# Kernel optimization log

Hardware: AMD Instinct MI355X
Metric: run time of the kernel (lower is better)

The kernel has to match this reference:

```python
import jax, jax.numpy as jnp
import numpy as np

B, Q, HID = 2, 2048, 2048
HQ, HKV, D = 16, 4, 128
EPS = 1e-6
THETA = 1000000.0


def _rmsnorm(x, w):
    # x: [..., D]
    return x * jax.lax.rsqrt(jnp.mean(x * x, axis=-1, keepdims=True) + EPS) * w


def _rope(x, cos, sin):
    # neox-style: split halves. x: [B,Q,H,D], cos/sin: [B,Q,1,D/2]
    d2 = x.shape[-1] // 2
    x1, x2 = x[..., :d2], x[..., d2:]
    return jnp.concatenate([x1 * cos - x2 * sin, x2 * cos + x1 * sin], axis=-1)


def setup_inputs() -> dict:
    key = jax.random.key(0)
    k1, k2, k3 = jax.random.split(key, 3)
    positions = jnp.broadcast_to(jnp.arange(Q, dtype=jnp.int32), (B, Q))
    hidden_states = jax.random.normal(k1, (B, Q, HID), dtype=jnp.float32)
    k_cache = jnp.zeros((B, HKV, Q, D), dtype=jnp.float32)
    v_cache = jnp.zeros((B, HKV, Q, D), dtype=jnp.float32)
    wqkv = jax.random.normal(k2, (HQ * D + 2 * HKV * D, HID), dtype=jnp.float32) * (HID ** -0.5)
    wo = jax.random.normal(k3, (HID, HQ * D), dtype=jnp.float32) * ((HQ * D) ** -0.5)
    q_norm_w = jnp.ones((D,), dtype=jnp.float32)
    k_norm_w = jnp.ones((D,), dtype=jnp.float32)
    return {"positions": positions, "hidden_states": hidden_states, "k_cache": k_cache,
            "v_cache": v_cache, "wqkv": wqkv, "wo": wo, "q_norm_w": q_norm_w,
            "k_norm_w": k_norm_w, "seq_len": Q}


def reference(positions, hidden_states, k_cache, v_cache, wqkv, wo, q_norm_w, k_norm_w, seq_len):
    bsz, qlen, _ = hidden_states.shape
    q_size, kv_size = HQ * D, HKV * D
    scale = D ** -0.5

    qkv = hidden_states.reshape(bsz * qlen, HID) @ wqkv.T  # [B*Q, q+2kv]
    q = qkv[:, :q_size].reshape(bsz, qlen, HQ, D)
    k = qkv[:, q_size:q_size + kv_size].reshape(bsz, qlen, HKV, D)
    v = qkv[:, q_size + kv_size:].reshape(bsz, qlen, HKV, D)

    q = _rmsnorm(q, q_norm_w)
    k = _rmsnorm(k, k_norm_w)

    inv_freq = 1.0 / (THETA ** (jnp.arange(0, D, 2, dtype=jnp.float32) / D))  # [D/2]
    freqs = positions.astype(jnp.float32)[..., None] * inv_freq  # [B,Q,D/2]
    cos = jnp.cos(freqs)[:, :, None, :]
    sin = jnp.sin(freqs)[:, :, None, :]
    q = _rope(q, cos, sin)
    k = _rope(k, cos, sin)

    q = q.transpose(0, 2, 1, 3)  # [B,HQ,Q,D]
    k = k.transpose(0, 2, 1, 3)  # [B,HKV,Q,D]
    v = v.transpose(0, 2, 1, 3)

    start = seq_len - qlen
    k_cache = jax.lax.dynamic_update_slice(k_cache, k, (0, 0, start, 0))
    v_cache = jax.lax.dynamic_update_slice(v_cache, v, (0, 0, start, 0))
    k_full = k_cache[:, :, :seq_len, :]
    v_full = v_cache[:, :, :seq_len, :]

    rep = HQ // HKV
    kf = jnp.repeat(k_full, rep, axis=1)  # [B,HQ,S,D]
    vf = jnp.repeat(v_full, rep, axis=1)

    scores = jnp.einsum('bhqd,bhkd->bhqk', q, kf) * scale
    if qlen == seq_len:  # is_causal path
        causal = jnp.tril(jnp.ones((qlen, seq_len), dtype=bool))
        scores = jnp.where(causal, scores, jnp.finfo(scores.dtype).min)
    attn = jax.nn.softmax(scores, axis=-1)
    out = jnp.einsum('bhqk,bhkd->bhqd', attn, vf)  # [B,HQ,Q,D]
    out = out.transpose(0, 2, 1, 3).reshape(bsz * qlen, HQ * D)
    return (out @ wo.T).reshape(bsz, qlen, HID)
```

## Files before the change

kernel.cpp:

```cpp
#include <hip/hip_runtime.h>

#define B_    2
#define Q_    2048
#define HID_  2048
#define HQ_   16
#define HKV_  4
#define D_    128
#define QSC_  (0.08838834764831843f * 1.4426950408889634f)
#define LOG2_THETA 19.931568569324174f
#define FMAX_ 20.0f

typedef unsigned short u16;
typedef __attribute__((ext_vector_type(8))) short bf16x8;
typedef __attribute__((ext_vector_type(4))) float f32x4;

__device__ __forceinline__ u16 f2bf(float x) {
  union { float f; unsigned int u; } v; v.f = x;
  unsigned int r = v.u + 0x7FFFu + ((v.u >> 16) & 1u);
  return (u16)(r >> 16);
}
__device__ __forceinline__ u16 f2bf_t(float x) {
  union { float f; unsigned int u; } v; v.f = x;
  return (u16)(v.u >> 16);
}

__device__ __forceinline__ void gl2lds16(u16* lds, const u16* g) {
  __builtin_amdgcn_global_load_lds((const __attribute__((address_space(1))) void*)g,
                                   (__attribute__((address_space(3))) void*)lds,
                                   16, 0, 0);
}

#define N4_HID  2097152
#define N4_WQKV 1572864
#define N4_WO   1048576
#define N4_ALL  (N4_HID + N4_WQKV + N4_WO)
#define NROPE   (B_ * Q_ * 64)
__global__ __launch_bounds__(256) void cvt_all(const float* __restrict__ h,
                                               const float* __restrict__ wq,
                                               const float* __restrict__ wo,
                                               const int* __restrict__ pos,
                                               u16* __restrict__ oh,
                                               u16* __restrict__ owq,
                                               u16* __restrict__ owo,
                                               float* __restrict__ rope) {
  int i = blockIdx.x * 256 + threadIdx.x;
  if (i >= N4_ALL) {
    int j = i - N4_ALL;
    int d = j & 63, row = j >> 6;
    float p = (float)pos[row];
    float inv = exp2f(-(float)d * (LOG2_THETA / 64.f));
    float sn, cn;
    sincosf(p * inv, &sn, &cn);
    ((float2*)rope)[j] = make_float2(cn, sn);
    return;
  }
  const float* src; u16* dst; int off;
  if (i < N4_HID)                 { src = h;  dst = oh;  off = i; }
  else if (i < N4_HID + N4_WQKV)  { src = wq; dst = owq; off = i - N4_HID; }
  else                            { src = wo; dst = owo; off = i - N4_HID - N4_WQKV; }
  float4 v = *(const float4*)(src + (size_t)off * 4);
  ushort4 o;
  o.x = f2bf(v.x); o.y = f2bf(v.y); o.z = f2bf(v.z); o.w = f2bf(v.w);
  *(ushort4*)(dst + (size_t)off * 4) = o;
}

__global__ __launch_bounds__(512) void gemm_qkv8(const u16* __restrict__ A,
                                                 const u16* __restrict__ Bw,
                                                 const float* __restrict__ rope,
                                                 const float* __restrict__ qw,
                                                 const float* __restrict__ kw,
                                                 u16* __restrict__ qb,
                                                 u16* __restrict__ kb,
                                                 u16* __restrict__ vt) {
  __shared__ __align__(16) u16 lds[65536];
  const int tid = threadIdx.x;
  const int wv = tid >> 6, lane = tid & 63;
  const int wm = wv >> 1, wn = wv & 1;
  const int c = lane & 15, quad = lane >> 4;
  const int m0 = blockIdx.x * 256;
  const int by = blockIdx.y;
  const int n0 = by * 256;
  const int xg = ((lane & 7) ^ (lane >> 3)) * 8;
  const int x0 = ((quad)     ^ (c & 7)) * 8;
  const int x1 = ((quad | 4) ^ (c & 7)) * 8;
  const int aoff = (wm >> 1) * 8192 + (wm & 1) * 4096 + c * 64;
  const int boff = 32768 + wn * 8192 + c * 64;
  const u16* Ag = A  + (size_t)m0 * HID_;
  const u16* Bg = Bw + (size_t)n0 * HID_;
  const int NIT = HID_ >> 7;

#define STGQ(base, g, h, kt, buf)                                             \
  { _Pragma("unroll")                                                         \
    for (int j = 0; j < 2; ++j) {                                             \
      const int s = j * 8 + wv;                                               \
      gl2lds16(lds + (base) + (buf) * 16384 + (h) * 8192 + s * 512,           \
               (g) + (size_t)((h) * 128 + s * 8 + (lane >> 3)) * HID_         \
                   + (kt) * 64 + xg);                                         \
    } }
#define STGQ_A(h, kt, buf) STGQ(0,     Ag, h, kt, buf)
#define STGQ_B(h, kt, buf) STGQ(32768, Bg, h, kt, buf)
#define BARQ()  asm volatile("s_barrier" ::: "memory")
#define WLGQ()  { asm volatile("s_waitcnt lgkmcnt(0)" ::: "memory");          \
                  __builtin_amdgcn_sched_barrier(0); }
#define WVMQ(n) { asm volatile("s_waitcnt vmcnt(" #n ")" ::: "memory");       \
                  __builtin_amdgcn_sched_barrier(0); }
#define MMQ(MF, NF, FA, MI) {                                                 \
  acc[MF][NF] = __builtin_amdgcn_mfma_f32_16x16x32_bf16(FA[MI][0], fB[(NF)&3][0], \
                                                        acc[MF][NF], 0, 0, 0);\
  acc[MF][NF] = __builtin_amdgcn_mfma_f32_16x16x32_bf16(FA[MI][1], fB[(NF)&3][1], \
                                                        acc[MF][NF], 0, 0, 0); }

  f32x4 acc[4][8] = {};
  bf16x8 fAa[2][2], fAb[2][2], fB[4][2];

  STGQ_A(0, 0, 0); STGQ_A(1, 0, 0); STGQ_B(0, 0, 0); STGQ_B(1, 0, 0);
  STGQ_A(0, 1, 1); STGQ_B(0, 1, 1);
  WVMQ(4);
  BARQ();

#pragma unroll 1
  for (int it = 0; it < NIT; ++it) {
    const bool last = (it == NIT - 1);
    const int kt1 = 2 * it + 1, kt2 = 2 * it + 2, kt3 = 2 * it + 3;

#pragma unroll
    for (int mi = 0; mi < 2; ++mi) {
      fAa[mi][0] = *(const bf16x8*)(lds + aoff + mi * 1024 + x0);
      fAa[mi][1] = *(const bf16x8*)(lds + aoff + mi * 1024 + x1);
    }
#pragma unroll
    for (int nf = 0; nf < 4; ++nf) {
      fB[nf][0] = *(const bf16x8*)(lds + boff + nf * 1024 + x0);
      fB[nf][1] = *(const bf16x8*)(lds + boff + nf * 1024 + x1);
    }
    STGQ_A(1, kt1, 1);
    BARQ(); WLGQ();
    __builtin_amdgcn_s_setprio(1);
#pragma unroll
    for (int mi = 0; mi < 2; ++mi)
#pragma unroll
      for (int nf = 0; nf < 4; ++nf) MMQ(mi, nf, fAa, mi);
    __builtin_amdgcn_s_setprio(0);
    BARQ();

#pragma unroll
    for (int mi = 0; mi < 2; ++mi) {
      fAb[mi][0] = *(const bf16x8*)(lds + aoff + (2 + mi) * 1024 + x0);
      fAb[mi][1] = *(const bf16x8*)(lds + aoff + (2 + mi) * 1024 + x1);
    }
    STGQ_B(1, kt1, 1);
    BARQ(); WLGQ();
    __builtin_amdgcn_s_setprio(1);
#pragma unroll
    for (int mi = 0; mi < 2; ++mi)
#pragma unroll
      for (int nf = 0; nf < 4; ++nf) MMQ(2 + mi, nf, fAb, mi);
    __builtin_amdgcn_s_setprio(0);
    BARQ();

#pragma unroll
    for (int nf = 0; nf < 4; ++nf) {
      fB[nf][0] = *(const bf16x8*)(lds + boff + (4 + nf) * 1024 + x0);
      fB[nf][1] = *(const bf16x8*)(lds + boff + (4 + nf) * 1024 + x1);
    }
    if (!last) STGQ_A(0, kt2, 0);
    BARQ(); WLGQ();
    __builtin_amdgcn_s_setprio(1);
#pragma unroll
    for (int mi = 0; mi < 2; ++mi)
#pragma unroll
      for (int nf = 4; nf < 8; ++nf) MMQ(2 + mi, nf, fAb, mi);
    __builtin_amdgcn_s_setprio(0);
    BARQ();

    if (!last) STGQ_B(0, kt2, 0);
    BARQ(); WLGQ();
    __builtin_amdgcn_s_setprio(1);
#pragma unroll
    for (int mi = 0; mi < 2; ++mi)
#pragma unroll
      for (int nf = 4; nf < 8; ++nf) MMQ(mi, nf, fAa, mi);
    __builtin_amdgcn_s_setprio(0);
    if (last) { WVMQ(0); } else { WVMQ(4); }
    BARQ();

#pragma unroll
    for (int mi = 0; mi < 2; ++mi) {
      fAa[mi][0] = *(const bf16x8*)(lds + 16384 + aoff + mi * 1024 + x0);
      fAa[mi][1] = *(const bf16x8*)(lds + 16384 + aoff + mi * 1024 + x1);
    }
#pragma unroll
    for (int nf = 0; nf < 4; ++nf) {
      fB[nf][0] = *(const bf16x8*)(lds + 16384 + boff + nf * 1024 + x0);
      fB[nf][1] = *(const bf16x8*)(lds + 16384 + boff + nf * 1024 + x1);
    }
    if (!last) STGQ_A(1, kt2, 0);
    BARQ(); WLGQ();
    __builtin_amdgcn_s_setprio(1);
#pragma unroll
    for (int mi = 0; mi < 2; ++mi)
#pragma unroll
      for (int nf = 0; nf < 4; ++nf) MMQ(mi, nf, fAa, mi);
    __builtin_amdgcn_s_setprio(0);
    BARQ();

#pragma unroll
    for (int mi = 0; mi < 2; ++mi) {
      fAb[mi][0] = *(const bf16x8*)(lds + 16384 + aoff + (2 + mi) * 1024 + x0);
      fAb[mi][1] = *(const bf16x8*)(lds + 16384 + aoff + (2 + mi) * 1024 + x1);
    }
    if (!last) STGQ_B(1, kt2, 0);
    BARQ(); WLGQ();
    __builtin_amdgcn_s_setprio(1);
#pragma unroll
    for (int mi = 0; mi < 2; ++mi)
#pragma unroll
      for (int nf = 0; nf < 4; ++nf) MMQ(2 + mi, nf, fAb, mi);
    __builtin_amdgcn_s_setprio(0);
    BARQ();

#pragma unroll
    for (int nf = 0; nf < 4; ++nf) {
      fB[nf][0] = *(const bf16x8*)(lds + 16384 + boff + (4 + nf) * 1024 + x0);
      fB[nf][1] = *(const bf16x8*)(lds + 16384 + boff + (4 + nf) * 1024 + x1);
    }
    if (!last) STGQ_A(0, kt3, 1);
    BARQ(); WLGQ();
    __builtin_amdgcn_s_setprio(1);
#pragma unroll
    for (int mi = 0; mi < 2; ++mi)
#pragma unroll
      for (int nf = 4; nf < 8; ++nf) MMQ(2 + mi, nf, fAb, mi);
    __builtin_amdgcn_s_setprio(0);
    BARQ();

    if (!last) STGQ_B(0, kt3, 1);
    BARQ(); WLGQ();
    __builtin_amdgcn_s_setprio(1);
#pragma unroll
    for (int mi = 0; mi < 2; ++mi)
#pragma unroll
      for (int nf = 4; nf < 8; ++nf) MMQ(mi, nf, fAa, mi);
    __builtin_amdgcn_s_setprio(0);
    if (last) { WVMQ(0); } else { WVMQ(4); }
    BARQ();
  }

  const int h = by * 2 + wn;
  if (h < 20) {
    const bool isq = h < 16;
    const float* w = isq ? qw : kw;
    const float osc = isq ? QSC_ : 1.f;
    float wl[8];
#pragma unroll
    for (int nf = 0; nf < 8; ++nf) wl[nf] = w[nf * 16 + c];
    u16* dstbuf = isq ? qb : kb;
    const int hbase = isq ? h : (h - 16);
    const int nheads = isq ? HQ_ : HKV_;
    u16* lw = lds + wv * 4224;
#pragma unroll
    for (int pass = 0; pass < 2; ++pass) {
#pragma unroll
      for (int mi = 0; mi < 2; ++mi) {
        const int mf = pass * 2 + mi;
#pragma unroll
        for (int r = 0; r < 4; ++r) {
          const int row = m0 + wm * 64 + mf * 16 + quad * 4 + r;
          const int q = row & (Q_ - 1), b = row >> 11;
          float ss = 0.f;
#pragma unroll
          for (int nf = 0; nf < 8; ++nf) ss += acc[mf][nf][r] * acc[mf][nf][r];
          ss += __shfl_xor(ss, 1); ss += __shfl_xor(ss, 2);
          ss += __shfl_xor(ss, 4); ss += __shfl_xor(ss, 8);
          const float rn = rsqrtf(ss * (1.f / 128.f) + 1e-6f) * osc;
          u16* lrow = lw + (mi * 16 + quad * 4 + r) * 132;
#pragma unroll
          for (int ni = 0; ni < 4; ni++) {
            float2 cssn = *(const float2*)(rope +
                ((size_t)(b * Q_ + q) * 64 + ni * 16 + c) * 2);
            float x1 = acc[mf][ni][r]     * wl[ni]     * rn;
            float x2 = acc[mf][ni + 4][r] * wl[ni + 4] * rn;
            lrow[ni * 16 + c]       = f2bf(x1 * cssn.x - x2 * cssn.y);
            lrow[(ni + 4) * 16 + c] = f2bf(x2 * cssn.x + x1 * cssn.y);
          }
        }
      }
#pragma unroll
      for (int itr = 0; itr < 8; ++itr) {
        const int rl = itr * 4 + quad;
        const int rowg = m0 + wm * 64 + pass * 32 + rl;
        const int q = rowg & (Q_ - 1), b = rowg >> 11;
        u16* dst = dstbuf + (((size_t)(b * nheads) + hbase) * Q_ + q) * D_ + c * 8;
        *(bf16x8*)dst = *(const bf16x8*)(lw + rl * 132 + c * 8);
      }
    }
  } else {
    const int hk = h - 20;
    const int bb = m0 >> 11;
    const int q0w = (m0 & (Q_ - 1)) + wm * 64;
    u16* lw = lds + wv * 4352;
#pragma unroll
    for (int pass = 0; pass < 2; ++pass) {
#pragma unroll
      for (int nfl = 0; nfl < 4; ++nfl) {
        const int nf = pass * 4 + nfl;
#pragma unroll
        for (int mf = 0; mf < 4; ++mf) {
          short4 pv;
          pv.x = (short)f2bf(acc[mf][nf][0]); pv.y = (short)f2bf(acc[mf][nf][1]);
          pv.z = (short)f2bf(acc[mf][nf][2]); pv.w = (short)f2bf(acc[mf][nf][3]);
          *(short4*)(lw + (nfl * 16 + c) * 68 + mf * 16 + quad * 4) = pv;
        }
      }
#pragma unroll
      for (int itr = 0; itr < 8; ++itr) {
        const int dl = itr * 8 + (lane >> 3);
        const int d = pass * 64 + dl;
        u16* dst = vt + (((size_t)(bb * HKV_) + hk) * D_ + d) * Q_ +
                   q0w + (lane & 7) * 8;
        *(bf16x8*)dst = *(const bf16x8*)(lw + dl * 68 + (lane & 7) * 8);
      }
    }
  }
#undef STGQ
#undef STGQ_A
#undef STGQ_B
#undef BARQ
#undef WLGQ
#undef WVMQ
#undef MMQ
}

__global__ __launch_bounds__(512) void gemm_bt8(const u16* __restrict__ A,
                                                const u16* __restrict__ Bw,
                                                float* __restrict__ C,
                                                int M, int N, int K) {
  __shared__ __align__(16) u16 lds[65536];
  const int tid = threadIdx.x;
  const int wv = tid >> 6, lane = tid & 63;
  const int wm = wv >> 2, wn = wv & 3;
  const int c = lane & 15, quad = lane >> 4;
  const int m0 = blockIdx.x * 256, n0 = blockIdx.y * 256;
  const int xg = ((lane & 7) ^ (lane >> 3)) * 8;
  const int x0 = ((quad)     ^ (c & 7)) * 8;
  const int x1 = ((quad | 4) ^ (c & 7)) * 8;
  const int aoff = wm * 8192 + c * 64;
  const int boff = 32768 + (wn >> 1) * 8192 + (wn & 1) * 4096 + c * 64;
  const u16* Ag = A  + (size_t)m0 * K;
  const u16* Bg = Bw + (size_t)n0 * K;
  const int NIT = K >> 7;

#define STG8(base, g, h, kt, buf)                                             \
  { _Pragma("unroll")                                                         \
    for (int j = 0; j < 2; ++j) {                                             \
      const int s = j * 8 + wv;                                               \
      gl2lds16(lds + (base) + (buf) * 16384 + (h) * 8192 + s * 512,           \
               (g) + (size_t)((h) * 128 + s * 8 + (lane >> 3)) * K            \
                   + (kt) * 64 + xg);                                         \
    } }
#define STG_A8(h, kt, buf) STG8(0,     Ag, h, kt, buf)
#define STG_B8(h, kt, buf) STG8(32768, Bg, h, kt, buf)
#define BAR8()  asm volatile("s_barrier" ::: "memory")
#define WLG8()  { asm volatile("s_waitcnt lgkmcnt(0)" ::: "memory");          \
                  __builtin_amdgcn_sched_barrier(0); }
#define WVM8(n) { asm volatile("s_waitcnt vmcnt(" #n ")" ::: "memory");       \
                  __builtin_amdgcn_sched_barrier(0); }
#define MFMA8(MF, NF, KS) acc[MF][NF] = __builtin_amdgcn_mfma_f32_16x16x32_bf16( \
                  fA[(MF) & 3][KS], fB[NF][KS], acc[MF][NF], 0, 0, 0)

  f32x4 acc[8][4] = {};
  bf16x8 fA[4][2], fB[4][2];

  STG_A8(0, 0, 0); STG_A8(1, 0, 0); STG_B8(0, 0, 0); STG_B8(1, 0, 0);
  STG_B8(0, 1, 1); STG_A8(0, 1, 1);
  WVM8(4);
  BAR8();

#pragma unroll 1
  for (int it = 0; it < NIT; ++it) {
    const bool last = (it == NIT - 1);
    const int kt1 = 2 * it + 1, kt2 = 2 * it + 2, kt3 = 2 * it + 3;

#pragma unroll
    for (int mf = 0; mf < 4; ++mf) {
      fA[mf][0] = *(const bf16x8*)(lds + aoff + mf * 1024 + x0);
      fA[mf][1] = *(const bf16x8*)(lds + aoff + mf * 1024 + x1);
    }
#pragma unroll
    for (int nf = 0; nf < 2; ++nf) {
      fB[nf][0] = *(const bf16x8*)(lds + boff + nf * 1024 + x0);
      fB[nf][1] = *(const bf16x8*)(lds + boff + nf * 1024 + x1);
    }
    STG_A8(1, kt1, 1);
    BAR8(); WLG8();
    __builtin_amdgcn_s_setprio(1);
#pragma unroll
    for (int mf = 0; mf < 4; ++mf)
#pragma unroll
      for (int nf = 0; nf < 2; ++nf) { MFMA8(mf, nf, 0); MFMA8(mf, nf, 1); }
    __builtin_amdgcn_s_setprio(0);
    BAR8();

#pragma unroll
    for (int nf = 2; nf < 4; ++nf) {
      fB[nf][0] = *(const bf16x8*)(lds + boff + nf * 1024 + x0);
      fB[nf][1] = *(const bf16x8*)(lds + boff + nf * 1024 + x1);
    }
    STG_B8(1, kt1, 1);
    BAR8(); WLG8();
    __builtin_amdgcn_s_setprio(1);
#pragma unroll
    for (int mf = 0; mf < 4; ++mf)
#pragma unroll
      for (int nf = 2; nf < 4; ++nf) { MFMA8(mf, nf, 0); MFMA8(mf, nf, 1); }
    __builtin_amdgcn_s_setprio(0);
    BAR8();

#pragma unroll
    for (int mf = 0; mf < 4; ++mf) {
      fA[mf][0] = *(const bf16x8*)(lds + aoff + (4 + mf) * 1024 + x0);
      fA[mf][1] = *(const bf16x8*)(lds + aoff + (4 + mf) * 1024 + x1);
    }
    if (!last) STG_B8(0, kt2, 0);
    BAR8(); WLG8();
    __builtin_amdgcn_s_setprio(1);
#pragma unroll
    for (int mf = 4; mf < 8; ++mf)
#pragma unroll
      for (int nf = 2; nf < 4; ++nf) { MFMA8(mf, nf, 0); MFMA8(mf, nf, 1); }
    __builtin_amdgcn_s_setprio(0);
    BAR8();

    if (!last) STG_A8(0, kt2, 0);
    BAR8(); WLG8();
    __builtin_amdgcn_s_setprio(1);
#pragma unroll
    for (int mf = 4; mf < 8; ++mf)
#pragma unroll
      for (int nf = 0; nf < 2; ++nf) { MFMA8(mf, nf, 0); MFMA8(mf, nf, 1); }
    __builtin_amdgcn_s_setprio(0);
    if (last) { WVM8(0); } else { WVM8(4); }
    BAR8();

#pragma unroll
    for (int mf = 0; mf < 4; ++mf) {
      fA[mf][0] = *(const bf16x8*)(lds + 16384 + aoff + mf * 1024 + x0);
      fA[mf][1] = *(const bf16x8*)(lds + 16384 + aoff + mf * 1024 + x1);
    }
#pragma unroll
    for (int nf = 0; nf < 2; ++nf) {
      fB[nf][0] = *(const bf16x8*)(lds + 16384 + boff + nf * 1024 + x0);
      fB[nf][1] = *(const bf16x8*)(lds + 16384 + boff + nf * 1024 + x1);
    }
    if (!last) STG_A8(1, kt2, 0);
    BAR8(); WLG8();
    __builtin_amdgcn_s_setprio(1);
#pragma unroll
    for (int mf = 0; mf < 4; ++mf)
#pragma unroll
      for (int nf = 0; nf < 2; ++nf) { MFMA8(mf, nf, 0); MFMA8(mf, nf, 1); }
    __builtin_amdgcn_s_setprio(0);
    BAR8();

#pragma unroll
    for (int nf = 2; nf < 4; ++nf) {
      fB[nf][0] = *(const bf16x8*)(lds + 16384 + boff + nf * 1024 + x0);
      fB[nf][1] = *(const bf16x8*)(lds + 16384 + boff + nf * 1024 + x1);
    }
    if (!last) STG_B8(1, kt2, 0);
    BAR8(); WLG8();
    __builtin_amdgcn_s_setprio(1);
#pragma unroll
    for (int mf = 0; mf < 4; ++mf)
#pragma unroll
      for (int nf = 2; nf < 4; ++nf) { MFMA8(mf, nf, 0); MFMA8(mf, nf, 1); }
    __builtin_amdgcn_s_setprio(0);
    BAR8();

#pragma unroll
    for (int mf = 0; mf < 4; ++mf) {
      fA[mf][0] = *(const bf16x8*)(lds + 16384 + aoff + (4 + mf) * 1024 + x0);
      fA[mf][1] = *(const bf16x8*)(lds + 16384 + aoff + (4 + mf) * 1024 + x1);
    }
    if (!last) STG_B8(0, kt3, 1);
    BAR8(); WLG8();
    __builtin_amdgcn_s_setprio(1);
#pragma unroll
    for (int mf = 4; mf < 8; ++mf)
#pragma unroll
      for (int nf = 2; nf < 4; ++nf) { MFMA8(mf, nf, 0); MFMA8(mf, nf, 1); }
    __builtin_amdgcn_s_setprio(0);
    BAR8();

    if (!last) STG_A8(0, kt3, 1);
    BAR8(); WLG8();
    __builtin_amdgcn_s_setprio(1);
#pragma unroll
    for (int mf = 4; mf < 8; ++mf)
#pragma unroll
      for (int nf = 0; nf < 2; ++nf) { MFMA8(mf, nf, 0); MFMA8(mf, nf, 1); }
    __builtin_amdgcn_s_setprio(0);
    if (last) { WVM8(0); } else { WVM8(4); }
    BAR8();
  }

  const int crow = m0 + wm * 128 + quad * 4;
  const int ccol = n0 + wn * 64 + c;
#pragma unroll
  for (int mf = 0; mf < 8; ++mf)
#pragma unroll
    for (int nf = 0; nf < 4; ++nf)
#pragma unroll
      for (int r = 0; r < 4; ++r)
        C[(size_t)(crow + mf * 16 + r) * N + ccol + nf * 16] = acc[mf][nf][r];
#undef STG8
#undef STG_A8
#undef STG_B8
#undef BAR8
#undef WLG8
#undef WVM8
#undef MFMA8
}

__global__ __launch_bounds__(256) void attn_fwd(const u16* __restrict__ qb,
                                                const u16* __restrict__ kb,
                                                const u16* __restrict__ vt,
                                                u16* __restrict__ ob) {
  __shared__ __align__(16) u16 lds[8192 + 8192 + 4608];
  u16* Ks = lds;
  u16* Vs = lds + 8192;
  u16* Ps = lds + 16384;
  const int p = blockIdx.x, h = blockIdx.y, b = blockIdx.z;
  const int hk = h >> 2;
  const int tid = threadIdx.x, wave = tid >> 6, lane = tid & 63;
  const int c = lane & 15, quad = lane >> 4;
  const int lr = lane >> 2, lp = lane & 3;
  const int lpg = (lp + 4 - ((lr >> 1) & 3)) & 3;
  const int swq = ((quad + (c >> 1)) & 3) * 8;
  const u16* qg = qb + ((size_t)b * HQ_ + h) * (size_t)Q_ * D_;
  const u16* kg = kb + ((size_t)b * HKV_ + hk) * (size_t)Q_ * D_;
  const u16* vg = vt + ((size_t)b * HKV_ + hk) * (size_t)D_ * Q_;
  u16* Pw = Ps + wave * 1152;
  u16* Bw = Ks + wave * 2176;

#pragma unroll 1
  for (int tp = 0; tp < 2; tp++) {
    const int t = tp ? (31 - p) : p;
    const int q0 = t * 64;
    const int qrow = q0 + wave * 16 + c;
    bf16x8 qf[4];
#pragma unroll
    for (int kk = 0; kk < 4; kk++)
      qf[kk] = *(const bf16x8*)(qg + (size_t)qrow * D_ + kk * 32 + quad * 8);
    f32x4 Oa[8] = {};
    float l_acc = 0.f;

#pragma unroll 1
    for (int kt = 0; kt <= t; kt++) {
      __syncthreads();
#pragma unroll
      for (int i = 0; i < 4; i++) {
        gl2lds16(Ks + (size_t)(i * 256 + wave * 64) * 8,
                 kg + ((size_t)kt * 64 + wave * 16 + lr) * D_ + i * 32 + lpg * 8);
        int d = (i & 1) * 64 + wave * 16 + lr;
        gl2lds16(Vs + (size_t)(i * 256 + wave * 64) * 8,
                 vg + (size_t)d * Q_ + kt * 64 + (i >> 1) * 32 + lpg * 8);
      }
      __syncthreads();
      f32x4 S[4];
#pragma unroll
      for (int n = 0; n < 4; n++) {
        f32x4 a = {-FMAX_, -FMAX_, -FMAX_, -FMAX_};
#pragma unroll
        for (int kk = 0; kk < 4; kk++) {
          bf16x8 kf = *(const bf16x8*)(Ks + kk * 2048 + (n * 16 + c) * 32 + swq);
          a = __builtin_amdgcn_mfma_f32_16x16x32_bf16(kf, qf[kk], a, 0, 0, 0);
        }
        S[n] = a;
      }
      if (kt == t) {
#pragma unroll
        for (int n = 0; n < 4; n++)
#pragma unroll
          for (int r = 0; r < 4; r++) {
            int key = kt * 64 + n * 16 + quad * 4 + r;
            if (key > qrow) S[n][r] = -1e9f;
          }
      }
#pragma unroll
      for (int n = 0; n < 4; n++) {
        float p0 = __builtin_amdgcn_exp2f(S[n][0]);
        float p1 = __builtin_amdgcn_exp2f(S[n][1]);
        float p2 = __builtin_amdgcn_exp2f(S[n][2]);
        float p3 = __builtin_amdgcn_exp2f(S[n][3]);
        l_acc += (p0 + p1) + (p2 + p3);
        short4 pk;
        pk.x = (short)f2bf_t(p0); pk.y = (short)f2bf_t(p1);
        pk.z = (short)f2bf_t(p2); pk.w = (short)f2bf_t(p3);
        *(short4*)(Pw + c * 72 + n * 16 + quad * 4) = pk;
      }
      bf16x8 pf[2];
#pragma unroll
      for (int kk2 = 0; kk2 < 2; kk2++)
        pf[kk2] = *(const bf16x8*)(Pw + c * 72 + kk2 * 32 + quad * 8);
#pragma unroll
      for (int md = 0; md < 8; md++)
#pragma unroll
        for (int kk2 = 0; kk2 < 2; kk2++) {
          bf16x8 vf = *(const bf16x8*)(Vs + kk2 * 4096 + (md * 16 + c) * 32 + swq);
          Oa[md] = __builtin_amdgcn_mfma_f32_16x16x32_bf16(vf, pf[kk2], Oa[md], 0, 0, 0);
        }
    }
    float l_row = l_acc;
    l_row += __shfl_xor(l_row, 16);
    l_row += __shfl_xor(l_row, 32);
    __syncthreads();
    const float invl = 1.f / l_row;
#pragma unroll
    for (int md = 0; md < 8; md++) {
      short4 ok;
      ok.x = (short)f2bf(Oa[md][0] * invl); ok.y = (short)f2bf(Oa[md][1] * invl);
      ok.z = (short)f2bf(Oa[md][2] * invl); ok.w = (short)f2bf(Oa[md][3] * invl);
      *(short4*)(Bw + c * 136 + md * 16 + quad * 4) = ok;
    }
    const int orow = q0 + wave * 16 + lr;
#pragma unroll
    for (int tt = 0; tt < 4; tt++) {
      bf16x8 ov = *(const bf16x8*)(Bw + lr * 136 + lp * 32 + tt * 8);
      *(bf16x8*)(ob + ((size_t)(b * Q_ + orow) * HQ_ + h) * D_ + lp * 32 + tt * 8) = ov;
    }
  }
}

extern "C" void kernel_launch(void* const* d_in, const int* in_sizes, int n_in,
                              void* d_out, int out_size, void* d_ws, size_t ws_size,
                              hipStream_t stream) {
  const int*   positions = (const int*)  d_in[0];
  const float* hidden    = (const float*)d_in[1];
  const float* wqkv      = (const float*)d_in[4];
  const float* wo        = (const float*)d_in[5];
  const float* qnw       = (const float*)d_in[6];
  const float* knw       = (const float*)d_in[7];
  char* ws = (char*)d_ws;
  u16*   hid_bf  = (u16*)(ws);
  u16*   wqkv_bf = (u16*)(ws + 16777216);
  u16*   wo_bf   = (u16*)(ws + 29360128);
  u16*   q_bf    = (u16*)(ws + 37748736);
  u16*   k_bf    = (u16*)(ws + 54525952);
  u16*   vt_bf   = (u16*)(ws + 58720256);
  float* rope    = (float*)(ws + 62914560);
  u16*   attn_bf = hid_bf;

  cvt_all<<<19456, 256, 0, stream>>>(hidden, wqkv, wo, positions,
                                     hid_bf, wqkv_bf, wo_bf, rope);
  gemm_qkv8<<<dim3(16, 12), 512, 0, stream>>>(hid_bf, wqkv_bf, rope, qnw, knw,
                                              q_bf, k_bf, vt_bf);
  attn_fwd<<<dim3(16, 16, 2), 256, 0, stream>>>(q_bf, k_bf, vt_bf, attn_bf);
  gemm_bt8<<<dim3(16, 8), 512, 0, stream>>>(attn_bf, wo_bf, (float*)d_out,
                                            4096, 2048, 2048);
}
```

Measured before the change: 309.1 us.

## Shrink output GEMM tile to 128x256 and double-buffer K/V loads in attention

The output projection GEMM moves from 256x256 tiles to 128x256 tiles, doubling the grid from 128 to 256 blocks so that more of the compute units have work. Its software pipeline is rebuilt with a smaller LDS footprint and split A/B fragment registers. The attention kernel now double-buffers its K and V tiles in LDS, prefetching the next tile while the current one is computed, which also removes one barrier per iteration. The cost is more LDS per attention block, which can lower occupancy, and less operand reuse per GEMM tile.

```diff
diff --git a/kernel.cpp b/kernel.cpp
--- a/kernel.cpp
+++ b/kernel.cpp
@@ -335,201 +335,173 @@
                                                 const u16* __restrict__ Bw,
                                                 float* __restrict__ C,
                                                 int M, int N, int K) {
-  __shared__ __align__(16) u16 lds[65536];
+  __shared__ __align__(16) u16 lds[49152];
   const int tid = threadIdx.x;
   const int wv = tid >> 6, lane = tid & 63;
   const int wm = wv >> 2, wn = wv & 3;
   const int c = lane & 15, quad = lane >> 4;
-  const int m0 = blockIdx.x * 256, n0 = blockIdx.y * 256;
+  const int m0 = blockIdx.x * 128, n0 = blockIdx.y * 256;
   const int xg = ((lane & 7) ^ (lane >> 3)) * 8;
   const int x0 = ((quad)     ^ (c & 7)) * 8;
   const int x1 = ((quad | 4) ^ (c & 7)) * 8;
-  const int aoff = wm * 8192 + c * 64;
-  const int boff = 32768 + (wn >> 1) * 8192 + (wn & 1) * 4096 + c * 64;
+  const int aoff = wm * 4096 + c * 64;
+  const int boff = 16384 + (wn >> 1) * 8192 + (wn & 1) * 4096 + c * 64;
   const u16* Ag = A  + (size_t)m0 * K;
   const u16* Bg = Bw + (size_t)n0 * K;
   const int NIT = K >> 7;
 
-#define STG8(base, g, h, kt, buf)                                             \
+#define STA2(h, kt, buf)                                                      \
+  gl2lds16(lds + (buf) * 8192 + (h) * 4096 + wv * 512,                        \
+           Ag + (size_t)((h) * 64 + wv * 8 + (lane >> 3)) * K + (kt) * 64 + xg);
+#define STB2(h, kt, buf)                                                      \
   { _Pragma("unroll")                                                         \
-    for (int j = 0; j < 2; ++j) {                                             \
-      const int s = j * 8 + wv;                                               \
-      gl2lds16(lds + (base) + (buf) * 16384 + (h) * 8192 + s * 512,           \
-               (g) + (size_t)((h) * 128 + s * 8 + (lane >> 3)) * K            \
-                   + (kt) * 64 + xg);                                         \
-    } }
-#define STG_A8(h, kt, buf) STG8(0,     Ag, h, kt, buf)
-#define STG_B8(h, kt, buf) STG8(32768, Bg, h, kt, buf)
+    for (int j = 0; j < 2; ++j)                                               \
+      gl2lds16(lds + 16384 + (buf) * 16384 + (h) * 8192 + j * 4096 + wv * 512,\
+               Bg + (size_t)((h) * 128 + j * 64 + wv * 8 + (lane >> 3)) * K   \
+                   + (kt) * 64 + xg); }
 #define BAR8()  asm volatile("s_barrier" ::: "memory")
 #define WLG8()  { asm volatile("s_waitcnt lgkmcnt(0)" ::: "memory");          \
                   __builtin_amdgcn_sched_barrier(0); }
 #define WVM8(n) { asm volatile("s_waitcnt vmcnt(" #n ")" ::: "memory");       \
                   __builtin_amdgcn_sched_barrier(0); }
-#define MFMA8(MF, NF, KS) acc[MF][NF] = __builtin_amdgcn_mfma_f32_16x16x32_bf16( \
-                  fA[(MF) & 3][KS], fB[NF][KS], acc[MF][NF], 0, 0, 0)
-
-  f32x4 acc[8][4] = {};
-  bf16x8 fA[4][2], fB[4][2];
-
-  STG_A8(0, 0, 0); STG_A8(1, 0, 0); STG_B8(0, 0, 0); STG_B8(1, 0, 0);
-  STG_B8(0, 1, 1); STG_A8(0, 1, 1);
-  WVM8(4);
+#define MM2(MF, NF, FA, FB, MI, NI) {                                         \
+  acc[MF][NF] = __builtin_amdgcn_mfma_f32_16x16x32_bf16(FA[MI][0], FB[NI][0], \
+                                                        acc[MF][NF], 0, 0, 0);\
+  acc[MF][NF] = __builtin_amdgcn_mfma_f32_16x16x32_bf16(FA[MI][1], FB[NI][1], \
+                                                        acc[MF][NF], 0, 0, 0); }
+
+  f32x4 acc[4][4] = {};
+  bf16x8 fAa[2][2], fAb[2][2], fBa[2][2], fBb[2][2];
+
+  STA2(0, 0, 0); STA2(1, 0, 0); STB2(0, 0, 0); STB2(1, 0, 0);
+  STA2(0, 1, 1); STA2(1, 1, 1); STB2(0, 1, 1); STB2(1, 1, 1);
+  WVM8(6);
   BAR8();
 
 #pragma unroll 1
   for (int it = 0; it < NIT; ++it) {
     const bool last = (it == NIT - 1);
-    const int kt1 = 2 * it + 1, kt2 = 2 * it + 2, kt3 = 2 * it + 3;
-
-#pragma unroll
-    for (int mf = 0; mf < 4; ++mf) {
-      fA[mf][0] = *(const bf16x8*)(lds + aoff + mf * 1024 + x0);
-      fA[mf][1] = *(const bf16x8*)(lds + aoff + mf * 1024 + x1);
-    }
-#pragma unroll
-    for (int nf = 0; nf < 2; ++nf) {
-      fB[nf][0] = *(const bf16x8*)(lds + boff + nf * 1024 + x0);
-      fB[nf][1] = *(const bf16x8*)(lds + boff + nf * 1024 + x1);
-    }
-    STG_A8(1, kt1, 1);
-    BAR8(); WLG8();
-    __builtin_amdgcn_s_setprio(1);
-#pragma unroll
-    for (int mf = 0; mf < 4; ++mf)
-#pragma unroll
-      for (int nf = 0; nf < 2; ++nf) { MFMA8(mf, nf, 0); MFMA8(mf, nf, 1); }
-    __builtin_amdgcn_s_setprio(0);
-    BAR8();
-
-#pragma unroll
-    for (int nf = 2; nf < 4; ++nf) {
-      fB[nf][0] = *(const bf16x8*)(lds + boff + nf * 1024 + x0);
-      fB[nf][1] = *(const bf16x8*)(lds + boff + nf * 1024 + x1);
-    }
-    STG_B8(1, kt1, 1);
-    BAR8(); WLG8();
-    __builtin_amdgcn_s_setprio(1);
-#pragma unroll
-    for (int mf = 0; mf < 4; ++mf)
-#pragma unroll
-      for (int nf = 2; nf < 4; ++nf) { MFMA8(mf, nf, 0); MFMA8(mf, nf, 1); }
-    __builtin_amdgcn_s_setprio(0);
-    BAR8();
-
-#pragma unroll
-    for (int mf = 0; mf < 4; ++mf) {
-      fA[mf][0] = *(const bf16x8*)(lds + aoff + (4 + mf) * 1024 + x0);
-      fA[mf][1] = *(const bf16x8*)(lds + aoff + (4 + mf) * 1024 + x1);
-    }
-    if (!last) STG_B8(0, kt2, 0);
-    BAR8(); WLG8();
-    __builtin_amdgcn_s_setprio(1);
-#pragma unroll
-    for (int mf = 4; mf < 8; ++mf)
-#pragma unroll
-      for (int nf = 2; nf < 4; ++nf) { MFMA8(mf, nf, 0); MFMA8(mf, nf, 1); }
-    __builtin_amdgcn_s_setprio(0);
-    BAR8();
-
-    if (!last) STG_A8(0, kt2, 0);
-    BAR8(); WLG8();
-    __builtin_amdgcn_s_setprio(1);
-#pragma unroll
-    for (int mf = 4; mf < 8; ++mf)
-#pragma unroll
-      for (int nf = 0; nf < 2; ++nf) { MFMA8(mf, nf, 0); MFMA8(mf, nf, 1); }
-    __builtin_amdgcn_s_setprio(0);
-    if (last) { WVM8(0); } else { WVM8(4); }
-    BAR8();
-
-#pragma unroll
-    for (int mf = 0; mf < 4; ++mf) {
-      fA[mf][0] = *(const bf16x8*)(lds + 16384 + aoff + mf * 1024 + x0);
-      fA[mf][1] = *(const bf16x8*)(lds + 16384 + aoff + mf * 1024 + x1);
-    }
-#pragma unroll
-    for (int nf = 0; nf < 2; ++nf) {
-      fB[nf][0] = *(const bf16x8*)(lds + 16384 + boff + nf * 1024 + x0);
-      fB[nf][1] = *(const bf16x8*)(lds + 16384 + boff + nf * 1024 + x1);
-    }
-    if (!last) STG_A8(1, kt2, 0);
-    BAR8(); WLG8();
-    __builtin_amdgcn_s_setprio(1);
-#pragma unroll
-    for (int mf = 0; mf < 4; ++mf)
-#pragma unroll
-      for (int nf = 0; nf < 2; ++nf) { MFMA8(mf, nf, 0); MFMA8(mf, nf, 1); }
-    __builtin_amdgcn_s_setprio(0);
-    BAR8();
-
-#pragma unroll
-    for (int nf = 2; nf < 4; ++nf) {
-      fB[nf][0] = *(const bf16x8*)(lds + 16384 + boff + nf * 1024 + x0);
-      fB[nf][1] = *(const bf16x8*)(lds + 16384 + boff + nf * 1024 + x1);
-    }
-    if (!last) STG_B8(1, kt2, 0);
-    BAR8(); WLG8();
-    __builtin_amdgcn_s_setprio(1);
-#pragma unroll
-    for (int mf = 0; mf < 4; ++mf)
-#pragma unroll
-      for (int nf = 2; nf < 4; ++nf) { MFMA8(mf, nf, 0); MFMA8(mf, nf, 1); }
-    __builtin_amdgcn_s_setprio(0);
-    BAR8();
-
-#pragma unroll
-    for (int mf = 0; mf < 4; ++mf) {
-      fA[mf][0] = *(const bf16x8*)(lds + 16384 + aoff + (4 + mf) * 1024 + x0);
-      fA[mf][1] = *(const bf16x8*)(lds + 16384 + aoff + (4 + mf) * 1024 + x1);
-    }
-    if (!last) STG_B8(0, kt3, 1);
-    BAR8(); WLG8();
-    __builtin_amdgcn_s_setprio(1);
-#pragma unroll
-    for (int mf = 4; mf < 8; ++mf)
-#pragma unroll
-      for (int nf = 2; nf < 4; ++nf) { MFMA8(mf, nf, 0); MFMA8(mf, nf, 1); }
-    __builtin_amdgcn_s_setprio(0);
-    BAR8();
-
-    if (!last) STG_A8(0, kt3, 1);
-    BAR8(); WLG8();
-    __builtin_amdgcn_s_setprio(1);
-#pragma unroll
-    for (int mf = 4; mf < 8; ++mf)
-#pragma unroll
-      for (int nf = 0; nf < 2; ++nf) { MFMA8(mf, nf, 0); MFMA8(mf, nf, 1); }
-    __builtin_amdgcn_s_setprio(0);
-    if (last) { WVM8(0); } else { WVM8(4); }
+    const int kt2 = 2 * it + 2, kt3 = 2 * it + 3;
+
+#pragma unroll
+    for (int mi = 0; mi < 2; ++mi) {
+      fAa[mi][0] = *(const bf16x8*)(lds + aoff + mi * 1024 + x0);
+      fAa[mi][1] = *(const bf16x8*)(lds + aoff + mi * 1024 + x1);
+      fBa[mi][0] = *(const bf16x8*)(lds + boff + mi * 1024 + x0);
+      fBa[mi][1] = *(const bf16x8*)(lds + boff + mi * 1024 + x1);
+    }
+    BAR8(); WLG8();
+    __builtin_amdgcn_s_setprio(1);
+    MM2(0, 0, fAa, fBa, 0, 0); MM2(0, 1, fAa, fBa, 0, 1);
+    MM2(1, 0, fAa, fBa, 1, 0); MM2(1, 1, fAa, fBa, 1, 1);
+    __builtin_amdgcn_s_setprio(0);
+    BAR8();
+
+#pragma unroll
+    for (int mi = 0; mi < 2; ++mi) {
+      fAb[mi][0] = *(const bf16x8*)(lds + aoff + (2 + mi) * 1024 + x0);
+      fAb[mi][1] = *(const bf16x8*)(lds + aoff + (2 + mi) * 1024 + x1);
+    }
+    BAR8(); WLG8();
+    __builtin_amdgcn_s_setprio(1);
+    MM2(2, 0, fAb, fBa, 0, 0); MM2(2, 1, fAb, fBa, 0, 1);
+    MM2(3, 0, fAb, fBa, 1, 0); MM2(3, 1, fAb, fBa, 1, 1);
+    __builtin_amdgcn_s_setprio(0);
+    BAR8();
+
+#pragma unroll
+    for (int ni = 0; ni < 2; ++ni) {
+      fBb[ni][0] = *(const bf16x8*)(lds + boff + (2 + ni) * 1024 + x0);
+      fBb[ni][1] = *(const bf16x8*)(lds + boff + (2 + ni) * 1024 + x1);
+    }
+    if (!last) { STA2(0, kt2, 0); STA2(1, kt2, 0); }
+    BAR8(); WLG8();
+    __builtin_amdgcn_s_setprio(1);
+    MM2(2, 2, fAb, fBb, 0, 0); MM2(2, 3, fAb, fBb, 0, 1);
+    MM2(3, 2, fAb, fBb, 1, 0); MM2(3, 3, fAb, fBb, 1, 1);
+    __builtin_amdgcn_s_setprio(0);
+    BAR8();
+
+    if (!last) { STB2(0, kt2, 0); STB2(1, kt2, 0); }
+    BAR8(); WLG8();
+    __builtin_amdgcn_s_setprio(1);
+    MM2(0, 2, fAa, fBb, 0, 0); MM2(0, 3, fAa, fBb, 0, 1);
+    MM2(1, 2, fAa, fBb, 1, 0); MM2(1, 3, fAa, fBb, 1, 1);
+    __builtin_amdgcn_s_setprio(0);
+    if (last) { WVM8(0); } else { WVM8(6); }
+    BAR8();
+
+#pragma unroll
+    for (int mi = 0; mi < 2; ++mi) {
+      fAa[mi][0] = *(const bf16x8*)(lds + 8192 + aoff + mi * 1024 + x0);
+      fAa[mi][1] = *(const bf16x8*)(lds + 8192 + aoff + mi * 1024 + x1);
+      fBa[mi][0] = *(const bf16x8*)(lds + 16384 + boff + mi * 1024 + x0);
+      fBa[mi][1] = *(const bf16x8*)(lds + 16384 + boff + mi * 1024 + x1);
+    }
+    BAR8(); WLG8();
+    __builtin_amdgcn_s_setprio(1);
+    MM2(0, 0, fAa, fBa, 0, 0); MM2(0, 1, fAa, fBa, 0, 1);
+    MM2(1, 0, fAa, fBa, 1, 0); MM2(1, 1, fAa, fBa, 1, 1);
+    __builtin_amdgcn_s_setprio(0);
+    BAR8();
+
+#pragma unroll
+    for (int mi = 0; mi < 2; ++mi) {
+      fAb[mi][0] = *(const bf16x8*)(lds + 8192 + aoff + (2 + mi) * 1024 + x0);
+      fAb[mi][1] = *(const bf16x8*)(lds + 8192 + aoff + (2 + mi) * 1024 + x1);
+    }
+    BAR8(); WLG8();
+    __builtin_amdgcn_s_setprio(1);
+    MM2(2, 0, fAb, fBa, 0, 0); MM2(2, 1, fAb, fBa, 0, 1);
+    MM2(3, 0, fAb, fBa, 1, 0); MM2(3, 1, fAb, fBa, 1, 1);
+    __builtin_amdgcn_s_setprio(0);
+    BAR8();
+
+#pragma unroll
+    for (int ni = 0; ni < 2; ++ni) {
+      fBb[ni][0] = *(const bf16x8*)(lds + 16384 + boff + (2 + ni) * 1024 + x0);
+      fBb[ni][1] = *(const bf16x8*)(lds + 16384 + boff + (2 + ni) * 1024 + x1);
+    }
+    if (!last) { STA2(0, kt3, 1); STA2(1, kt3, 1); }
+    BAR8(); WLG8();
+    __builtin_amdgcn_s_setprio(1);
+    MM2(2, 2, fAb, fBb, 0, 0); MM2(2, 3, fAb, fBb, 0, 1);
+    MM2(3, 2, fAb, fBb, 1, 0); MM2(3, 3, fAb, fBb, 1, 1);
+    __builtin_amdgcn_s_setprio(0);
+    BAR8();
+
+    if (!last) { STB2(0, kt3, 1); STB2(1, kt3, 1); }
+    BAR8(); WLG8();
+    __builtin_amdgcn_s_setprio(1);
+    MM2(0, 2, fAa, fBb, 0, 0); MM2(0, 3, fAa, fBb, 0, 1);
+    MM2(1, 2, fAa, fBb, 1, 0); MM2(1, 3, fAa, fBb, 1, 1);
+    __builtin_amdgcn_s_setprio(0);
+    if (last) { WVM8(0); } else { WVM8(6); }
     BAR8();
   }
 
-  const int crow = m0 + wm * 128 + quad * 4;
+  const int crow = m0 + wm * 64 + quad * 4;
   const int ccol = n0 + wn * 64 + c;
 #pragma unroll
-  for (int mf = 0; mf < 8; ++mf)
+  for (int mf = 0; mf < 4; ++mf)
 #pragma unroll
     for (int nf = 0; nf < 4; ++nf)
 #pragma unroll
       for (int r = 0; r < 4; ++r)
         C[(size_t)(crow + mf * 16 + r) * N + ccol + nf * 16] = acc[mf][nf][r];
-#undef STG8
-#undef STG_A8
-#undef STG_B8
+#undef STA2
+#undef STB2
 #undef BAR8
 #undef WLG8
 #undef WVM8
-#undef MFMA8
+#undef MM2
 }
 
 __global__ __launch_bounds__(256) void attn_fwd(const u16* __restrict__ qb,
                                                 const u16* __restrict__ kb,
                                                 const u16* __restrict__ vt,
                                                 u16* __restrict__ ob) {
-  __shared__ __align__(16) u16 lds[8192 + 8192 + 4608];
-  u16* Ks = lds;
-  u16* Vs = lds + 8192;
-  u16* Ps = lds + 16384;
+  __shared__ __align__(16) u16 lds[2 * 8192 + 2 * 8192 + 4608];
   const int p = blockIdx.x, h = blockIdx.y, b = blockIdx.z;
   const int hk = h >> 2;
   const int tid = threadIdx.x, wave = tid >> 6, lane = tid & 63;
@@ -540,8 +512,18 @@
   const u16* qg = qb + ((size_t)b * HQ_ + h) * (size_t)Q_ * D_;
   const u16* kg = kb + ((size_t)b * HKV_ + hk) * (size_t)Q_ * D_;
   const u16* vg = vt + ((size_t)b * HKV_ + hk) * (size_t)D_ * Q_;
-  u16* Pw = Ps + wave * 1152;
-  u16* Bw = Ks + wave * 2176;
+  u16* Pw = lds + 32768 + wave * 1152;
+  u16* Bw = lds + wave * 2176;
+
+#define ASTAGE(KT, BS)                                                        \
+  { _Pragma("unroll")                                                         \
+    for (int i = 0; i < 4; i++) {                                             \
+      gl2lds16(lds + (BS) * 8192 + (size_t)(i * 256 + wave * 64) * 8,         \
+               kg + ((size_t)(KT) * 64 + wave * 16 + lr) * D_ + i * 32 + lpg * 8); \
+      int d = (i & 1) * 64 + wave * 16 + lr;                                  \
+      gl2lds16(lds + 16384 + (BS) * 8192 + (size_t)(i * 256 + wave * 64) * 8, \
+               vg + (size_t)d * Q_ + (KT) * 64 + (i >> 1) * 32 + lpg * 8);    \
+    } }
 
 #pragma unroll 1
   for (int tp = 0; tp < 2; tp++) {
@@ -555,25 +537,23 @@
     f32x4 Oa[8] = {};
     float l_acc = 0.f;
 
+    if (tp) __syncthreads();
+    ASTAGE(0, 0);
+
 #pragma unroll 1
     for (int kt = 0; kt <= t; kt++) {
+      const int bs = kt & 1;
       __syncthreads();
-#pragma unroll
-      for (int i = 0; i < 4; i++) {
-        gl2lds16(Ks + (size_t)(i * 256 + wave * 64) * 8,
-                 kg + ((size_t)kt * 64 + wave * 16 + lr) * D_ + i * 32 + lpg * 8);
-        int d = (i & 1) * 64 + wave * 16 + lr;
-        gl2lds16(Vs + (size_t)(i * 256 + wave * 64) * 8,
-                 vg + (size_t)d * Q_ + kt * 64 + (i >> 1) * 32 + lpg * 8);
-      }
-      __syncthreads();
+      if (kt < t) ASTAGE(kt + 1, bs ^ 1);
+      const u16* Ksb = lds + bs * 8192;
+      const u16* Vsb = lds + 16384 + bs * 8192;
       f32x4 S[4];
 #pragma unroll
       for (int n = 0; n < 4; n++) {
         f32x4 a = {-FMAX_, -FMAX_, -FMAX_, -FMAX_};
 #pragma unroll
         for (int kk = 0; kk < 4; kk++) {
-          bf16x8 kf = *(const bf16x8*)(Ks + kk * 2048 + (n * 16 + c) * 32 + swq);
+          bf16x8 kf = *(const bf16x8*)(Ksb + kk * 2048 + (n * 16 + c) * 32 + swq);
           a = __builtin_amdgcn_mfma_f32_16x16x32_bf16(kf, qf[kk], a, 0, 0, 0);
         }
         S[n] = a;
@@ -607,7 +587,7 @@
       for (int md = 0; md < 8; md++)
 #pragma unroll
         for (int kk2 = 0; kk2 < 2; kk2++) {
-          bf16x8 vf = *(const bf16x8*)(Vs + kk2 * 4096 + (md * 16 + c) * 32 + swq);
+          bf16x8 vf = *(const bf16x8*)(Vsb + kk2 * 4096 + (md * 16 + c) * 32 + swq);
           Oa[md] = __builtin_amdgcn_mfma_f32_16x16x32_bf16(vf, pf[kk2], Oa[md], 0, 0, 0);
         }
     }
@@ -630,6 +610,7 @@
       *(bf16x8*)(ob + ((size_t)(b * Q_ + orow) * HQ_ + h) * D_ + lp * 32 + tt * 8) = ov;
     }
   }
+#undef ASTAGE
 }
 
 extern "C" void kernel_launch(void* const* d_in, const int* in_sizes, int n_in,
@@ -656,6 +637,6 @@
   gemm_qkv8<<<dim3(16, 12), 512, 0, stream>>>(hid_bf, wqkv_bf, rope, qnw, knw,
                                               q_bf, k_bf, vt_bf);
   attn_fwd<<<dim3(16, 16, 2), 256, 0, stream>>>(q_bf, k_bf, vt_bf, attn_bf);
-  gemm_bt8<<<dim3(16, 8), 512, 0, stream>>>(attn_bf, wo_bf, (float*)d_out,
+  gemm_bt8<<<dim3(32, 8), 512, 0, stream>>>(attn_bf, wo_bf, (float*)d_out,
                                             4096, 2048, 2048);
 }
```

Result: faster. 281.5 us (-8.9%).
